# Kernel optimization log

Measured on AMD Instinct MI355X. Metric: run time of the kernel, lower is better.

Reference implementation:

```python
import jax, jax.numpy as jnp
import numpy as np

B, L, D = 2, 1024, 1024
HID, E, K = 2048, 8, 2

def setup_inputs() -> dict:
    key = jax.random.key(0)
    ks = jax.random.split(key, 4)
    std = 0.02
    return {
        "x": jax.random.normal(ks[0], (B, L, D), dtype=jnp.float32),
        "router_scale": jnp.ones((D,), dtype=jnp.float32),
        "router_w": jax.random.normal(ks[1], (D, E), dtype=jnp.float32) * std,
        "gating_w": jax.random.normal(ks[2], (E, 2, HID, D), dtype=jnp.float32) * std,
        "linear_w": jax.random.normal(ks[3], (E, HID, D), dtype=jnp.float32) * std,
        "per_expert_scale": jnp.ones((E,), dtype=jnp.float32),
    }

def reference(x, router_scale, router_w, gating_w, linear_w, per_expert_scale):
    d = x.shape[-1]
    # RMSNorm without scale
    var = jnp.mean(jnp.square(x), axis=-1, keepdims=True)
    r_in = x * jax.lax.rsqrt(var + 1e-6)
    r_in = r_in * jax.lax.rsqrt(jnp.array(d, dtype=r_in.dtype)) * router_scale
    # Router
    logits = jnp.dot(r_in, router_w).astype(jnp.float32)          # [B,L,E]
    probs = jax.nn.softmax(logits, axis=-1)
    _, top_k_idx = jax.lax.top_k(logits, K)                        # [B,L,K]
    indicator = jax.nn.one_hot(top_k_idx, probs.shape[-1], dtype=probs.dtype)  # [B,L,K,E]
    gate_weights = indicator.sum(axis=-2) * probs                  # [B,L,E]
    renorm = jnp.sum(gate_weights, axis=-1, keepdims=True)
    renorm = jnp.where(renorm > 0.0, renorm, 1.0)
    weights = probs / renorm
    top_k_w = jnp.take_along_axis(weights, top_k_idx, axis=-1)     # [B,L,K]
    # Combine weights per expert (indices in top-k are distinct)
    combine = jnp.einsum('blke,blk->ble', indicator, top_k_w)      # [B,L,E]
    combine = combine * per_expert_scale                            # fold per-expert scale
    # Dense all-expert GELU-gated FFN; identical math to per-token gathered weights,
    # since unselected experts get combine weight 0.
    gate0 = jnp.einsum('bld,ehd->bleh', x, gating_w[:, 0])         # [B,L,E,H]
    gate1 = jnp.einsum('bld,ehd->bleh', x, gating_w[:, 1])
    act = jax.nn.gelu(gate0) * gate1                               # approximate gelu, as flax nn.gelu
    out = jnp.einsum('bleh,ehd,ble->bld', act, linear_w, combine)
    return out.astype(x.dtype)
```

## Files before the change

### kernel.cpp

```cpp
#include <hip/hip_runtime.h>
#include <math.h>

#define NB 2
#define NL 1024
#define ND 1024
#define NH 2048
#define NE 8
#define NTOK (NB*NL)
#define NSLOT (NTOK*2)

typedef float f32x4 __attribute__((ext_vector_type(4)));
typedef short s16x8 __attribute__((ext_vector_type(8)));
typedef short s16x4 __attribute__((ext_vector_type(4)));
typedef unsigned u32x4 __attribute__((ext_vector_type(4)));

__device__ __forceinline__ unsigned short f2bf(float f) {
    union { float f; unsigned u; } v; v.f = f;
    unsigned r = v.u + 0x7FFFu + ((v.u >> 16) & 1u);
    return (unsigned short)(r >> 16);
}

__device__ __forceinline__ unsigned pk2(float a, float b) {
    unsigned r;
    asm("v_cvt_pk_bf16_f32 %0, %1, %2" : "=v"(r) : "v"(a), "v"(b));
    return r;
}

__device__ __forceinline__ void gl_lds16(const unsigned short* g, unsigned short* l) {
    __builtin_amdgcn_global_load_lds(
        (const __attribute__((address_space(1))) unsigned int*)(const void*)g,
        (__attribute__((address_space(3))) unsigned int*)(void*)l, 16, 0, 0);
}

__global__ void router_kernel(const float* __restrict__ x,
                              const float* __restrict__ rscale,
                              const float* __restrict__ rw,
                              const float* __restrict__ pes,
                              int* __restrict__ cursor,
                              int* __restrict__ tok_slot,
                              float* __restrict__ w_slot,
                              unsigned short* __restrict__ xb)
{
    const int wave = threadIdx.x >> 6;
    const int lane = threadIdx.x & 63;
    const int t = blockIdx.x * 4 + wave;
    const float* xt = x + (size_t)t * ND;
    unsigned short* xbt = xb + (size_t)t * ND;

    float part[NE];
#pragma unroll
    for (int e = 0; e < NE; ++e) part[e] = 0.f;
    float ss = 0.f;

#pragma unroll
    for (int i = 0; i < 4; ++i) {
        int d = (lane + 64 * i) * 4;
        float4 xv = *(const float4*)(xt + d);
        float4 sv = *(const float4*)(rscale + d);
        s16x4 o;
        o[0] = (short)f2bf(xv.x); o[1] = (short)f2bf(xv.y);
        o[2] = (short)f2bf(xv.z); o[3] = (short)f2bf(xv.w);
        *(s16x4*)(xbt + d) = o;
        float xs[4] = {xv.x, xv.y, xv.z, xv.w};
        float sc[4] = {sv.x, sv.y, sv.z, sv.w};
        const float* rwp = rw + (size_t)d * NE;
#pragma unroll
        for (int c = 0; c < 4; ++c) {
            float v = xs[c];
            ss += v * v;
            float xr = v * sc[c];
            float4 r0 = *(const float4*)(rwp + c * NE);
            float4 r1 = *(const float4*)(rwp + c * NE + 4);
            part[0] += xr * r0.x; part[1] += xr * r0.y;
            part[2] += xr * r0.z; part[3] += xr * r0.w;
            part[4] += xr * r1.x; part[5] += xr * r1.y;
            part[6] += xr * r1.z; part[7] += xr * r1.w;
        }
    }
#pragma unroll
    for (int off = 32; off > 0; off >>= 1) {
        ss += __shfl_xor(ss, off, 64);
#pragma unroll
        for (int e = 0; e < NE; ++e) part[e] += __shfl_xor(part[e], off, 64);
    }
    if (lane == 0) {
        float rinv = rsqrtf(ss * (1.f / ND) + 1e-6f) * rsqrtf((float)ND);
        float lg[NE];
#pragma unroll
        for (int e = 0; e < NE; ++e) lg[e] = part[e] * rinv;
        int i0 = 0; float b0 = lg[0];
#pragma unroll
        for (int e = 1; e < NE; ++e) if (lg[e] > b0) { b0 = lg[e]; i0 = e; }
        int i1 = -1; float b1 = -INFINITY;
#pragma unroll
        for (int e = 0; e < NE; ++e) if (e != i0 && lg[e] > b1) { b1 = lg[e]; i1 = e; }
        float e1 = expf(b1 - b0);
        float denom = 1.f + e1;
        float w0 = pes[i0] / denom;
        float w1 = pes[i1] * e1 / denom;
        int s0 = atomicAdd(&cursor[i0], 1);
        tok_slot[i0 * NTOK + s0] = t; w_slot[i0 * NTOK + s0] = w0;
        int s1 = atomicAdd(&cursor[i1], 1);
        tok_slot[i1 * NTOK + s1] = t; w_slot[i1 * NTOK + s1] = w1;
    }
}

#define TL_BLOCKS ((ND/64)*(NH/64)*NE)
__global__ __launch_bounds__(256) void prep_weights(const float* __restrict__ lw,
                                                    unsigned short* __restrict__ lwT)
{
    const int b2 = blockIdx.x;
    const int tid = threadIdx.x;
    const int d0 = (b2 & 15) * 64;
    const int h0 = ((b2 >> 4) & 31) * 64;
    const int e  = b2 >> 9;
    __shared__ unsigned short T[64][66];
    {
        const int hr = tid >> 2;
        const int dc = (tid & 3) * 16;
        const float* p = lw + ((size_t)e * NH + h0 + hr) * ND + d0 + dc;
        float t[16];
        *(float4*)&t[0]  = *(const float4*)(p);
        *(float4*)&t[4]  = *(const float4*)(p + 4);
        *(float4*)&t[8]  = *(const float4*)(p + 8);
        *(float4*)&t[12] = *(const float4*)(p + 12);
#pragma unroll
        for (int i = 0; i < 8; ++i) {
            unsigned pk = (unsigned)f2bf(t[2 * i]) | ((unsigned)f2bf(t[2 * i + 1]) << 16);
            *(unsigned*)&T[hr][dc + 2 * i] = pk;
        }
    }
    __syncthreads();
    {
        const int dr = tid >> 2;
        const int hc = (tid & 3) * 16;
        s16x8 o0, o1;
#pragma unroll
        for (int i = 0; i < 8; ++i) o0[i] = (short)T[hc + i][dr];
#pragma unroll
        for (int i = 0; i < 8; ++i) o1[i] = (short)T[hc + 8 + i][dr];
        unsigned short* q = lwT + ((size_t)e * ND + d0 + dr) * NH + h0 + hc;
        *(s16x8*)(q)     = o0;
        *(s16x8*)(q + 8) = o1;
    }
}

#define BM 128
#define BH 64
#define BK 32
__global__ __launch_bounds__(256, 3) void gate_gemm(
    const unsigned short* __restrict__ xb, const float* __restrict__ gw,
    const int* __restrict__ cursor,
    const int* __restrict__ tok_slot, const float* __restrict__ w_slot,
    unsigned short* __restrict__ act)
{
    const int e = blockIdx.z;
    const int n = cursor[e];
    const int row0 = blockIdx.y * BM;
    if (row0 >= n) return;
    const int b0 = e * NTOK;
    const int h0 = blockIdx.x * BH;

    __shared__ unsigned short As[BM][BK];
    __shared__ unsigned short Bs[BM][BK];
    __shared__ int toks[BM];
    __shared__ float swv[BM];

    const int tid = threadIdx.x;
    if (tid < BM) {
        int r = row0 + tid;
        toks[tid] = (r < n) ? tok_slot[b0 + r] : 0;
        swv[tid]  = (r < n) ? w_slot[b0 + r] : 0.f;
    }
    __syncthreads();

    const int lane = tid & 63;
    const int wid  = tid >> 6;
    const int wm = wid & 1;
    const int wn = wid >> 1;

    const int drow = lane >> 2;
    const int c8  = (((lane & 3) - ((lane >> 3) & 3)) & 3) * 8;
    const int ar0 = wid * 32 + drow;
    const unsigned short* asrc0 = xb + (size_t)toks[ar0] * ND + c8;
    const unsigned short* asrc1 = xb + (size_t)toks[ar0 + 16] * ND + c8;
    const int br0 = wid * 32 + drow;
    const int br1 = br0 + 16;
    const float* bsrc0 = gw + (((size_t)e * 2 + (br0 >> 6)) * NH + h0 + (br0 & 63)) * ND + c8;
    const float* bsrc1 = gw + (((size_t)e * 2 + (br1 >> 6)) * NH + h0 + (br1 & 63)) * ND + c8;
    unsigned short* bdst0 = &Bs[br0][(lane & 3) * 8];
    unsigned short* bdst1 = &Bs[br1][(lane & 3) * 8];

    f32x4 acc[2][4][2];
#pragma unroll
    for (int gg = 0; gg < 2; ++gg)
#pragma unroll
        for (int i = 0; i < 4; ++i)
#pragma unroll
            for (int j = 0; j < 2; ++j)
                acc[gg][i][j] = (f32x4){0.f, 0.f, 0.f, 0.f};

    const int fr = lane & 15;
    const int pS = (((lane >> 4) + (fr >> 1)) & 3) * 8;

    for (int k0 = 0; k0 < ND; k0 += BK) {
        f32x4 b00 = *(const f32x4*)(bsrc0 + k0);
        f32x4 b01 = *(const f32x4*)(bsrc0 + k0 + 4);
        f32x4 b10 = *(const f32x4*)(bsrc1 + k0);
        f32x4 b11 = *(const f32x4*)(bsrc1 + k0 + 4);
        gl_lds16(asrc0 + k0, &As[wid * 32][0]);
        gl_lds16(asrc1 + k0, &As[wid * 32 + 16][0]);
        u32x4 w0, w1;
        w0[0] = pk2(b00[0], b00[1]); w0[1] = pk2(b00[2], b00[3]);
        w0[2] = pk2(b01[0], b01[1]); w0[3] = pk2(b01[2], b01[3]);
        w1[0] = pk2(b10[0], b10[1]); w1[1] = pk2(b10[2], b10[3]);
        w1[2] = pk2(b11[0], b11[1]); w1[3] = pk2(b11[2], b11[3]);
        *(u32x4*)bdst0 = w0;
        *(u32x4*)bdst1 = w1;
        __syncthreads();

        s16x8 af[4], bfr[2][2];
#pragma unroll
        for (int i = 0; i < 4; ++i)
            af[i] = *(const s16x8*)&As[wm * 64 + i * 16 + fr][pS];
#pragma unroll
        for (int gg = 0; gg < 2; ++gg)
#pragma unroll
            for (int j = 0; j < 2; ++j)
                bfr[gg][j] = *(const s16x8*)&Bs[gg * 64 + wn * 32 + j * 16 + fr][pS];
#pragma unroll
        for (int gg = 0; gg < 2; ++gg)
#pragma unroll
            for (int i = 0; i < 4; ++i)
#pragma unroll
                for (int j = 0; j < 2; ++j)
                    acc[gg][i][j] = __builtin_amdgcn_mfma_f32_16x16x32_bf16(
                        af[i], bfr[gg][j], acc[gg][i][j], 0, 0, 0);
        __syncthreads();
    }

    const int rb = (lane >> 4) * 4;
#pragma unroll
    for (int i = 0; i < 4; ++i)
#pragma unroll
        for (int r = 0; r < 4; ++r) {
            int ml = wm * 64 + i * 16 + rb + r;
            int rr = row0 + ml;
            if (rr < n) {
                float w = swv[ml];
#pragma unroll
                for (int j = 0; j < 2; ++j) {
                    float g0v = acc[0][i][j][r];
                    float g1v = acc[1][i][j][r];
                    float u = 0.7978845608028654f * (g0v + 0.044715f * g0v * g0v * g0v);
                    float ex = __expf(2.f * u);
                    float th = 1.f - 2.f / (ex + 1.f);
                    float a = 0.5f * g0v * (1.f + th) * g1v * w;
                    act[(size_t)(b0 + rr) * NH + (h0 + wn * 32 + j * 16 + fr)] = f2bf(a);
                }
            }
        }
}

#define DBM 128
#define DBN 128
#define DBK 32
#define KSPLIT 2
#define KC (NH / KSPLIT)
__global__ __launch_bounds__(256, 3) void down_gemm(
    const unsigned short* __restrict__ act, const unsigned short* __restrict__ lwT,
    const int* __restrict__ cursor,
    const int* __restrict__ tok_slot, float* __restrict__ out)
{
    const int e  = blockIdx.z >> 1;
    const int kc = blockIdx.z & 1;
    const int n = cursor[e];
    const int row0 = blockIdx.y * DBM;
    if (row0 >= n) return;
    const int b0 = e * NTOK;
    const int d0 = blockIdx.x * DBN;

    __shared__ unsigned short As[DBM][DBK];
    __shared__ unsigned short Bs[DBN][DBK];
    __shared__ int stok[DBM];

    const int tid = threadIdx.x;
    if (tid < DBM) {
        int r = row0 + tid;
        stok[tid] = (r < n) ? tok_slot[b0 + r] : 0;
    }
    __syncthreads();

    const int lane = tid & 63;
    const int wid  = tid >> 6;
    const int wm = wid & 1;
    const int wn = wid >> 1;

    const int drow = lane >> 2;
    const int c8  = (((lane & 3) - ((lane >> 3) & 3)) & 3) * 8;
    const int ar0 = wid * 32 + drow;
    const int rr0 = row0 + ar0, rr1 = rr0 + 16;
    const int sl0 = b0 + (rr0 < n ? rr0 : 0);
    const int sl1 = b0 + (rr1 < n ? rr1 : 0);
    const unsigned short* asrc0 = act + (size_t)sl0 * NH + kc * KC + c8;
    const unsigned short* asrc1 = act + (size_t)sl1 * NH + kc * KC + c8;
    const unsigned short* bsrc0 = lwT + ((size_t)e * ND + d0 + ar0) * NH + kc * KC + c8;
    const unsigned short* bsrc1 = bsrc0 + 16 * NH;

    f32x4 acc[4][4];
#pragma unroll
    for (int i = 0; i < 4; ++i)
#pragma unroll
        for (int j = 0; j < 4; ++j)
            acc[i][j] = (f32x4){0.f, 0.f, 0.f, 0.f};

    const int fr = lane & 15;
    const int pS = (((lane >> 4) + (fr >> 1)) & 3) * 8;

    for (int k0 = 0; k0 < KC; k0 += DBK) {
        gl_lds16(asrc0 + k0, &As[wid * 32][0]);
        gl_lds16(asrc1 + k0, &As[wid * 32 + 16][0]);
        gl_lds16(bsrc0 + k0, &Bs[wid * 32][0]);
        gl_lds16(bsrc1 + k0, &Bs[wid * 32 + 16][0]);
        __syncthreads();

        s16x8 af[4], bfr[4];
#pragma unroll
        for (int i = 0; i < 4; ++i)
            af[i] = *(const s16x8*)&As[wm * 64 + i * 16 + fr][pS];
#pragma unroll
        for (int j = 0; j < 4; ++j)
            bfr[j] = *(const s16x8*)&Bs[wn * 64 + j * 16 + fr][pS];
#pragma unroll
        for (int i = 0; i < 4; ++i)
#pragma unroll
            for (int j = 0; j < 4; ++j)
                acc[i][j] = __builtin_amdgcn_mfma_f32_16x16x32_bf16(af[i], bfr[j], acc[i][j], 0, 0, 0);
        __syncthreads();
    }

    const int rb = (lane >> 4) * 4;
#pragma unroll
    for (int i = 0; i < 4; ++i)
#pragma unroll
        for (int r = 0; r < 4; ++r) {
            int ml = wm * 64 + i * 16 + rb + r;
            int rr = row0 + ml;
            if (rr < n) {
                int tok = stok[ml];
#pragma unroll
                for (int j = 0; j < 4; ++j)
                    atomicAdd(&out[(size_t)tok * ND + d0 + wn * 64 + j * 16 + fr],
                              acc[i][j][r]);
            }
        }
}

extern "C" void kernel_launch(void* const* d_in, const int* in_sizes, int n_in,
                              void* d_out, int out_size, void* d_ws, size_t ws_size,
                              hipStream_t stream)
{
    const float* x      = (const float*)d_in[0];
    const float* rscale = (const float*)d_in[1];
    const float* rw     = (const float*)d_in[2];
    const float* gw     = (const float*)d_in[3];
    const float* lw     = (const float*)d_in[4];
    const float* pes    = (const float*)d_in[5];
    float* out = (float*)d_out;

    char* ws = (char*)d_ws;
    int* cursor = (int*)ws;
    int*   tok_slot      = (int*)(ws + 128);
    float* w_slot        = (float*)(ws + 65664);
    unsigned short* xb   = (unsigned short*)(ws + 131200);
    unsigned short* act  = (unsigned short*)(ws + 4325504);
    unsigned short* lwT  = (unsigned short*)(ws + 71434368);

    hipMemsetAsync(d_ws, 0, 128, stream);
    hipMemsetAsync(d_out, 0, (size_t)out_size * sizeof(float), stream);

    router_kernel<<<NTOK / 4, 256, 0, stream>>>(x, rscale, rw, pes, cursor,
                                                tok_slot, w_slot, xb);

    prep_weights<<<TL_BLOCKS, 256, 0, stream>>>(lw, lwT);

    dim3 g2(NH / BH, NTOK / BM, NE);
    gate_gemm<<<g2, 256, 0, stream>>>(xb, gw, cursor, tok_slot, w_slot, act);

    dim3 g3(ND / DBN, NTOK / DBM, NE * KSPLIT);
    down_gemm<<<g3, 256, 0, stream>>>(act, lwT, cursor, tok_slot, out);
}
```

Baseline: 429.8 us.

## Double-buffer LDS tiles in gate and down GEMMs to overlap loads with MFMA

Both grouped GEMM kernels now keep two LDS buffers for the A and B tiles. The next K-tile is fetched (global-to-LDS for activations, register-staged fp32-to-bf16 conversion for gate weights) while the MFMAs run on the current tile, which removes one barrier per iteration. Launch bounds are raised from 3 to 4 waves per SIMD to push occupancy. The cost is doubled LDS use and more register pressure, which may limit achievable occupancy or cause spills.

```diff
diff --git a/kernel.cpp b/kernel.cpp
--- a/kernel.cpp
+++ b/kernel.cpp
@@ -148,7 +148,7 @@
 #define BM 128
 #define BH 64
 #define BK 32
-__global__ __launch_bounds__(256, 3) void gate_gemm(
+__global__ __launch_bounds__(256, 4) void gate_gemm(
     const unsigned short* __restrict__ xb, const float* __restrict__ gw,
     const int* __restrict__ cursor,
     const int* __restrict__ tok_slot, const float* __restrict__ w_slot,
@@ -161,8 +161,8 @@
     const int b0 = e * NTOK;
     const int h0 = blockIdx.x * BH;
 
-    __shared__ unsigned short As[BM][BK];
-    __shared__ unsigned short Bs[BM][BK];
+    __shared__ unsigned short As[2][BM][BK];
+    __shared__ unsigned short Bs[2][BM][BK];
     __shared__ int toks[BM];
     __shared__ float swv[BM];
 
@@ -188,8 +188,7 @@
     const int br1 = br0 + 16;
     const float* bsrc0 = gw + (((size_t)e * 2 + (br0 >> 6)) * NH + h0 + (br0 & 63)) * ND + c8;
     const float* bsrc1 = gw + (((size_t)e * 2 + (br1 >> 6)) * NH + h0 + (br1 & 63)) * ND + c8;
-    unsigned short* bdst0 = &Bs[br0][(lane & 3) * 8];
-    unsigned short* bdst1 = &Bs[br1][(lane & 3) * 8];
+    const int bc = (lane & 3) * 8;
 
     f32x4 acc[2][4][2];
 #pragma unroll
@@ -203,31 +202,50 @@
     const int fr = lane & 15;
     const int pS = (((lane >> 4) + (fr >> 1)) & 3) * 8;
 
-    for (int k0 = 0; k0 < ND; k0 += BK) {
-        f32x4 b00 = *(const f32x4*)(bsrc0 + k0);
-        f32x4 b01 = *(const f32x4*)(bsrc0 + k0 + 4);
-        f32x4 b10 = *(const f32x4*)(bsrc1 + k0);
-        f32x4 b11 = *(const f32x4*)(bsrc1 + k0 + 4);
-        gl_lds16(asrc0 + k0, &As[wid * 32][0]);
-        gl_lds16(asrc1 + k0, &As[wid * 32 + 16][0]);
+    const int NT = ND / BK;
+
+    {
+        f32x4 b00 = *(const f32x4*)(bsrc0);
+        f32x4 b01 = *(const f32x4*)(bsrc0 + 4);
+        f32x4 b10 = *(const f32x4*)(bsrc1);
+        f32x4 b11 = *(const f32x4*)(bsrc1 + 4);
+        gl_lds16(asrc0, &As[0][wid * 32][0]);
+        gl_lds16(asrc1, &As[0][wid * 32 + 16][0]);
         u32x4 w0, w1;
         w0[0] = pk2(b00[0], b00[1]); w0[1] = pk2(b00[2], b00[3]);
         w0[2] = pk2(b01[0], b01[1]); w0[3] = pk2(b01[2], b01[3]);
         w1[0] = pk2(b10[0], b10[1]); w1[1] = pk2(b10[2], b10[3]);
         w1[2] = pk2(b11[0], b11[1]); w1[3] = pk2(b11[2], b11[3]);
-        *(u32x4*)bdst0 = w0;
-        *(u32x4*)bdst1 = w1;
-        __syncthreads();
+        *(u32x4*)&Bs[0][br0][bc] = w0;
+        *(u32x4*)&Bs[0][br1][bc] = w1;
+    }
+    __syncthreads();
+
+    for (int t = 0; t < NT; ++t) {
+        const int cur = t & 1;
+        const int nxt = cur ^ 1;
+        const int k1 = (t + 1) * BK;
+        const bool more = (t + 1 < NT);
+
+        f32x4 n00, n01, n10, n11;
+        if (more) {
+            n00 = *(const f32x4*)(bsrc0 + k1);
+            n01 = *(const f32x4*)(bsrc0 + k1 + 4);
+            n10 = *(const f32x4*)(bsrc1 + k1);
+            n11 = *(const f32x4*)(bsrc1 + k1 + 4);
+            gl_lds16(asrc0 + k1, &As[nxt][wid * 32][0]);
+            gl_lds16(asrc1 + k1, &As[nxt][wid * 32 + 16][0]);
+        }
 
         s16x8 af[4], bfr[2][2];
 #pragma unroll
         for (int i = 0; i < 4; ++i)
-            af[i] = *(const s16x8*)&As[wm * 64 + i * 16 + fr][pS];
+            af[i] = *(const s16x8*)&As[cur][wm * 64 + i * 16 + fr][pS];
 #pragma unroll
         for (int gg = 0; gg < 2; ++gg)
 #pragma unroll
             for (int j = 0; j < 2; ++j)
-                bfr[gg][j] = *(const s16x8*)&Bs[gg * 64 + wn * 32 + j * 16 + fr][pS];
+                bfr[gg][j] = *(const s16x8*)&Bs[cur][gg * 64 + wn * 32 + j * 16 + fr][pS];
 #pragma unroll
         for (int gg = 0; gg < 2; ++gg)
 #pragma unroll
@@ -236,6 +254,16 @@
                 for (int j = 0; j < 2; ++j)
                     acc[gg][i][j] = __builtin_amdgcn_mfma_f32_16x16x32_bf16(
                         af[i], bfr[gg][j], acc[gg][i][j], 0, 0, 0);
+
+        if (more) {
+            u32x4 w0, w1;
+            w0[0] = pk2(n00[0], n00[1]); w0[1] = pk2(n00[2], n00[3]);
+            w0[2] = pk2(n01[0], n01[1]); w0[3] = pk2(n01[2], n01[3]);
+            w1[0] = pk2(n10[0], n10[1]); w1[1] = pk2(n10[2], n10[3]);
+            w1[2] = pk2(n11[0], n11[1]); w1[3] = pk2(n11[2], n11[3]);
+            *(u32x4*)&Bs[nxt][br0][bc] = w0;
+            *(u32x4*)&Bs[nxt][br1][bc] = w1;
+        }
         __syncthreads();
     }
 
@@ -267,7 +295,7 @@
 #define DBK 32
 #define KSPLIT 2
 #define KC (NH / KSPLIT)
-__global__ __launch_bounds__(256, 3) void down_gemm(
+__global__ __launch_bounds__(256, 4) void down_gemm(
     const unsigned short* __restrict__ act, const unsigned short* __restrict__ lwT,
     const int* __restrict__ cursor,
     const int* __restrict__ tok_slot, float* __restrict__ out)
@@ -280,8 +308,8 @@
     const int b0 = e * NTOK;
     const int d0 = blockIdx.x * DBN;
 
-    __shared__ unsigned short As[DBM][DBK];
-    __shared__ unsigned short Bs[DBN][DBK];
+    __shared__ unsigned short As[2][DBM][DBK];
+    __shared__ unsigned short Bs[2][DBN][DBK];
     __shared__ int stok[DBM];
 
     const int tid = threadIdx.x;
@@ -317,20 +345,32 @@
     const int fr = lane & 15;
     const int pS = (((lane >> 4) + (fr >> 1)) & 3) * 8;
 
-    for (int k0 = 0; k0 < KC; k0 += DBK) {
-        gl_lds16(asrc0 + k0, &As[wid * 32][0]);
-        gl_lds16(asrc1 + k0, &As[wid * 32 + 16][0]);
-        gl_lds16(bsrc0 + k0, &Bs[wid * 32][0]);
-        gl_lds16(bsrc1 + k0, &Bs[wid * 32 + 16][0]);
-        __syncthreads();
+    const int NT = KC / DBK;
+
+    gl_lds16(asrc0, &As[0][wid * 32][0]);
+    gl_lds16(asrc1, &As[0][wid * 32 + 16][0]);
+    gl_lds16(bsrc0, &Bs[0][wid * 32][0]);
+    gl_lds16(bsrc1, &Bs[0][wid * 32 + 16][0]);
+    __syncthreads();
+
+    for (int t = 0; t < NT; ++t) {
+        const int cur = t & 1;
+        const int nxt = cur ^ 1;
+        const int k1 = (t + 1) * DBK;
+        if (t + 1 < NT) {
+            gl_lds16(asrc0 + k1, &As[nxt][wid * 32][0]);
+            gl_lds16(asrc1 + k1, &As[nxt][wid * 32 + 16][0]);
+            gl_lds16(bsrc0 + k1, &Bs[nxt][wid * 32][0]);
+            gl_lds16(bsrc1 + k1, &Bs[nxt][wid * 32 + 16][0]);
+        }
 
         s16x8 af[4], bfr[4];
 #pragma unroll
         for (int i = 0; i < 4; ++i)
-            af[i] = *(const s16x8*)&As[wm * 64 + i * 16 + fr][pS];
+            af[i] = *(const s16x8*)&As[cur][wm * 64 + i * 16 + fr][pS];
 #pragma unroll
         for (int j = 0; j < 4; ++j)
-            bfr[j] = *(const s16x8*)&Bs[wn * 64 + j * 16 + fr][pS];
+            bfr[j] = *(const s16x8*)&Bs[cur][wn * 64 + j * 16 + fr][pS];
 #pragma unroll
         for (int i = 0; i < 4; ++i)
 #pragma unroll
```

After: 418.4 us. 2.7% less time.

## Double-buffer LDS in both expert GEMMs and replace atomics with partial-sum gather

Applied to the files above, without the earlier changes.

Both gate and down GEMMs switch from direct global-to-LDS loads with a single buffer to register-staged, double-buffered LDS tiles, so global loads for the next K tile overlap MFMA work on the current one. The down GEMM no longer atomically adds into the output. It writes per-slot, per-K-split partial results into a workspace buffer, and a new gather kernel sums the four partials per token using a token-to-slot map recorded by the router. This removes the output memset and the float atomics, at the cost of extra register pressure, a larger workspace (about 128 MB of partials), and an additional launch.

```diff
diff --git a/kernel.cpp b/kernel.cpp
--- a/kernel.cpp
+++ b/kernel.cpp
@@ -26,12 +26,6 @@
     return r;
 }
 
-__device__ __forceinline__ void gl_lds16(const unsigned short* g, unsigned short* l) {
-    __builtin_amdgcn_global_load_lds(
-        (const __attribute__((address_space(1))) unsigned int*)(const void*)g,
-        (__attribute__((address_space(3))) unsigned int*)(void*)l, 16, 0, 0);
-}
-
 __global__ void router_kernel(const float* __restrict__ x,
                               const float* __restrict__ rscale,
                               const float* __restrict__ rw,
@@ -39,6 +33,7 @@
                               int* __restrict__ cursor,
                               int* __restrict__ tok_slot,
                               float* __restrict__ w_slot,
+                              int2* __restrict__ t2s,
                               unsigned short* __restrict__ xb)
 {
     const int wave = threadIdx.x >> 6;
@@ -102,6 +97,7 @@
         tok_slot[i0 * NTOK + s0] = t; w_slot[i0 * NTOK + s0] = w0;
         int s1 = atomicAdd(&cursor[i1], 1);
         tok_slot[i1 * NTOK + s1] = t; w_slot[i1 * NTOK + s1] = w1;
+        t2s[t] = make_int2(i0 * NTOK + s0, i1 * NTOK + s1);
     }
 }
 
@@ -148,6 +144,48 @@
 #define BM 128
 #define BH 64
 #define BK 32
+
+#define G_ISSUE(Sa0,Sa1,Sb0,Sb1,Sb2,Sb3,k) do { \
+    Sa0 = *(const s16x8*)(asrc0 + (k)); \
+    Sa1 = *(const s16x8*)(asrc1 + (k)); \
+    Sb0 = *(const f32x4*)(bsrc0 + (k)); \
+    Sb1 = *(const f32x4*)(bsrc0 + (k) + 4); \
+    Sb2 = *(const f32x4*)(bsrc1 + (k)); \
+    Sb3 = *(const f32x4*)(bsrc1 + (k) + 4); \
+} while(0)
+
+#define G_WRITE(P,Sa0,Sa1,Sb0,Sb1,Sb2,Sb3) do { \
+    *(s16x8*)&As[P][arow][acol]      = Sa0; \
+    *(s16x8*)&As[P][arow + 16][acol] = Sa1; \
+    u32x4 w0_, w1_; \
+    w0_[0] = pk2(Sb0[0],Sb0[1]); w0_[1] = pk2(Sb0[2],Sb0[3]); \
+    w0_[2] = pk2(Sb1[0],Sb1[1]); w0_[3] = pk2(Sb1[2],Sb1[3]); \
+    w1_[0] = pk2(Sb2[0],Sb2[1]); w1_[1] = pk2(Sb2[2],Sb2[3]); \
+    w1_[2] = pk2(Sb3[0],Sb3[1]); w1_[3] = pk2(Sb3[2],Sb3[3]); \
+    *(u32x4*)&Bs[P][arow][acol]      = w0_; \
+    *(u32x4*)&Bs[P][arow + 16][acol] = w1_; \
+} while(0)
+
+#define G_COMPUTE(P) do { \
+    s16x8 af[4], bfr[2][2]; \
+    _Pragma("unroll") \
+    for (int i_ = 0; i_ < 4; ++i_) \
+        af[i_] = *(const s16x8*)&As[P][wm * 64 + i_ * 16 + fr][pS]; \
+    _Pragma("unroll") \
+    for (int g_ = 0; g_ < 2; ++g_) \
+        _Pragma("unroll") \
+        for (int j_ = 0; j_ < 2; ++j_) \
+            bfr[g_][j_] = *(const s16x8*)&Bs[P][g_ * 64 + wn * 32 + j_ * 16 + fr][pS]; \
+    _Pragma("unroll") \
+    for (int g_ = 0; g_ < 2; ++g_) \
+        _Pragma("unroll") \
+        for (int i_ = 0; i_ < 4; ++i_) \
+            _Pragma("unroll") \
+            for (int j_ = 0; j_ < 2; ++j_) \
+                acc[g_][i_][j_] = __builtin_amdgcn_mfma_f32_16x16x32_bf16( \
+                    af[i_], bfr[g_][j_], acc[g_][i_][j_], 0, 0, 0); \
+} while(0)
+
 __global__ __launch_bounds__(256, 3) void gate_gemm(
     const unsigned short* __restrict__ xb, const float* __restrict__ gw,
     const int* __restrict__ cursor,
@@ -161,8 +199,8 @@
     const int b0 = e * NTOK;
     const int h0 = blockIdx.x * BH;
 
-    __shared__ unsigned short As[BM][BK];
-    __shared__ unsigned short Bs[BM][BK];
+    __shared__ unsigned short As[2][BM][BK];
+    __shared__ unsigned short Bs[2][BM][BK];
     __shared__ int toks[BM];
     __shared__ float swv[BM];
 
@@ -181,15 +219,13 @@
 
     const int drow = lane >> 2;
     const int c8  = (((lane & 3) - ((lane >> 3) & 3)) & 3) * 8;
-    const int ar0 = wid * 32 + drow;
-    const unsigned short* asrc0 = xb + (size_t)toks[ar0] * ND + c8;
-    const unsigned short* asrc1 = xb + (size_t)toks[ar0 + 16] * ND + c8;
-    const int br0 = wid * 32 + drow;
-    const int br1 = br0 + 16;
-    const float* bsrc0 = gw + (((size_t)e * 2 + (br0 >> 6)) * NH + h0 + (br0 & 63)) * ND + c8;
+    const int arow = wid * 32 + drow;
+    const int acol = (lane & 3) * 8;
+    const unsigned short* asrc0 = xb + (size_t)toks[arow] * ND + c8;
+    const unsigned short* asrc1 = xb + (size_t)toks[arow + 16] * ND + c8;
+    const int br1 = arow + 16;
+    const float* bsrc0 = gw + (((size_t)e * 2 + (arow >> 6)) * NH + h0 + (arow & 63)) * ND + c8;
     const float* bsrc1 = gw + (((size_t)e * 2 + (br1 >> 6)) * NH + h0 + (br1 & 63)) * ND + c8;
-    unsigned short* bdst0 = &Bs[br0][(lane & 3) * 8];
-    unsigned short* bdst1 = &Bs[br1][(lane & 3) * 8];
 
     f32x4 acc[2][4][2];
 #pragma unroll
@@ -203,39 +239,24 @@
     const int fr = lane & 15;
     const int pS = (((lane >> 4) + (fr >> 1)) & 3) * 8;
 
-    for (int k0 = 0; k0 < ND; k0 += BK) {
-        f32x4 b00 = *(const f32x4*)(bsrc0 + k0);
-        f32x4 b01 = *(const f32x4*)(bsrc0 + k0 + 4);
-        f32x4 b10 = *(const f32x4*)(bsrc1 + k0);
-        f32x4 b11 = *(const f32x4*)(bsrc1 + k0 + 4);
-        gl_lds16(asrc0 + k0, &As[wid * 32][0]);
-        gl_lds16(asrc1 + k0, &As[wid * 32 + 16][0]);
-        u32x4 w0, w1;
-        w0[0] = pk2(b00[0], b00[1]); w0[1] = pk2(b00[2], b00[3]);
-        w0[2] = pk2(b01[0], b01[1]); w0[3] = pk2(b01[2], b01[3]);
-        w1[0] = pk2(b10[0], b10[1]); w1[1] = pk2(b10[2], b10[3]);
-        w1[2] = pk2(b11[0], b11[1]); w1[3] = pk2(b11[2], b11[3]);
-        *(u32x4*)bdst0 = w0;
-        *(u32x4*)bdst1 = w1;
+    const int NT = ND / BK;
+
+    s16x8 xa0, xa1, ya0, ya1;
+    f32x4 xb0, xb1, xb2, xb3, yb0, yb1, yb2, yb3;
+
+    G_ISSUE(xa0, xa1, xb0, xb1, xb2, xb3, 0);
+    G_ISSUE(ya0, ya1, yb0, yb1, yb2, yb3, BK);
+    G_WRITE(0, xa0, xa1, xb0, xb1, xb2, xb3);
+    __syncthreads();
+
+    for (int t = 0; t < NT; t += 2) {
+        if (t + 2 < NT) G_ISSUE(xa0, xa1, xb0, xb1, xb2, xb3, (t + 2) * BK);
+        G_COMPUTE(0);
+        G_WRITE(1, ya0, ya1, yb0, yb1, yb2, yb3);
         __syncthreads();
-
-        s16x8 af[4], bfr[2][2];
-#pragma unroll
-        for (int i = 0; i < 4; ++i)
-            af[i] = *(const s16x8*)&As[wm * 64 + i * 16 + fr][pS];
-#pragma unroll
-        for (int gg = 0; gg < 2; ++gg)
-#pragma unroll
-            for (int j = 0; j < 2; ++j)
-                bfr[gg][j] = *(const s16x8*)&Bs[gg * 64 + wn * 32 + j * 16 + fr][pS];
-#pragma unroll
-        for (int gg = 0; gg < 2; ++gg)
-#pragma unroll
-            for (int i = 0; i < 4; ++i)
-#pragma unroll
-                for (int j = 0; j < 2; ++j)
-                    acc[gg][i][j] = __builtin_amdgcn_mfma_f32_16x16x32_bf16(
-                        af[i], bfr[gg][j], acc[gg][i][j], 0, 0, 0);
+        if (t + 3 < NT) G_ISSUE(ya0, ya1, yb0, yb1, yb2, yb3, (t + 3) * BK);
+        G_COMPUTE(1);
+        if (t + 2 < NT) G_WRITE(0, xa0, xa1, xb0, xb1, xb2, xb3);
         __syncthreads();
     }
 
@@ -267,10 +288,41 @@
 #define DBK 32
 #define KSPLIT 2
 #define KC (NH / KSPLIT)
+
+#define D_ISSUE(Sa0,Sa1,Sb0,Sb1,k) do { \
+    Sa0 = *(const s16x8*)(asrc0 + (k)); \
+    Sa1 = *(const s16x8*)(asrc1 + (k)); \
+    Sb0 = *(const s16x8*)(bsrc0 + (k)); \
+    Sb1 = *(const s16x8*)(bsrc1 + (k)); \
+} while(0)
+
+#define D_WRITE(P,Sa0,Sa1,Sb0,Sb1) do { \
+    *(s16x8*)&As[P][arow][acol]      = Sa0; \
+    *(s16x8*)&As[P][arow + 16][acol] = Sa1; \
+    *(s16x8*)&Bs[P][arow][acol]      = Sb0; \
+    *(s16x8*)&Bs[P][arow + 16][acol] = Sb1; \
+} while(0)
+
+#define D_COMPUTE(P) do { \
+    s16x8 af[4], bfr[4]; \
+    _Pragma("unroll") \
+    for (int i_ = 0; i_ < 4; ++i_) \
+        af[i_] = *(const s16x8*)&As[P][wm * 64 + i_ * 16 + fr][pS]; \
+    _Pragma("unroll") \
+    for (int j_ = 0; j_ < 4; ++j_) \
+        bfr[j_] = *(const s16x8*)&Bs[P][wn * 64 + j_ * 16 + fr][pS]; \
+    _Pragma("unroll") \
+    for (int i_ = 0; i_ < 4; ++i_) \
+        _Pragma("unroll") \
+        for (int j_ = 0; j_ < 4; ++j_) \
+            acc[i_][j_] = __builtin_amdgcn_mfma_f32_16x16x32_bf16( \
+                af[i_], bfr[j_], acc[i_][j_], 0, 0, 0); \
+} while(0)
+
 __global__ __launch_bounds__(256, 3) void down_gemm(
     const unsigned short* __restrict__ act, const unsigned short* __restrict__ lwT,
     const int* __restrict__ cursor,
-    const int* __restrict__ tok_slot, float* __restrict__ out)
+    const int* __restrict__ tok_slot, float* __restrict__ partial)
 {
     const int e  = blockIdx.z >> 1;
     const int kc = blockIdx.z & 1;
@@ -280,17 +332,10 @@
     const int b0 = e * NTOK;
     const int d0 = blockIdx.x * DBN;
 
-    __shared__ unsigned short As[DBM][DBK];
-    __shared__ unsigned short Bs[DBN][DBK];
-    __shared__ int stok[DBM];
+    __shared__ unsigned short As[2][DBM][DBK];
+    __shared__ unsigned short Bs[2][DBN][DBK];
 
     const int tid = threadIdx.x;
-    if (tid < DBM) {
-        int r = row0 + tid;
-        stok[tid] = (r < n) ? tok_slot[b0 + r] : 0;
-    }
-    __syncthreads();
-
     const int lane = tid & 63;
     const int wid  = tid >> 6;
     const int wm = wid & 1;
@@ -298,13 +343,14 @@
 
     const int drow = lane >> 2;
     const int c8  = (((lane & 3) - ((lane >> 3) & 3)) & 3) * 8;
-    const int ar0 = wid * 32 + drow;
-    const int rr0 = row0 + ar0, rr1 = rr0 + 16;
+    const int arow = wid * 32 + drow;
+    const int acol = (lane & 3) * 8;
+    const int rr0 = row0 + arow, rr1 = rr0 + 16;
     const int sl0 = b0 + (rr0 < n ? rr0 : 0);
     const int sl1 = b0 + (rr1 < n ? rr1 : 0);
     const unsigned short* asrc0 = act + (size_t)sl0 * NH + kc * KC + c8;
     const unsigned short* asrc1 = act + (size_t)sl1 * NH + kc * KC + c8;
-    const unsigned short* bsrc0 = lwT + ((size_t)e * ND + d0 + ar0) * NH + kc * KC + c8;
+    const unsigned short* bsrc0 = lwT + ((size_t)e * ND + d0 + arow) * NH + kc * KC + c8;
     const unsigned short* bsrc1 = bsrc0 + 16 * NH;
 
     f32x4 acc[4][4];
@@ -317,28 +363,29 @@
     const int fr = lane & 15;
     const int pS = (((lane >> 4) + (fr >> 1)) & 3) * 8;
 
-    for (int k0 = 0; k0 < KC; k0 += DBK) {
-        gl_lds16(asrc0 + k0, &As[wid * 32][0]);
-        gl_lds16(asrc1 + k0, &As[wid * 32 + 16][0]);
-        gl_lds16(bsrc0 + k0, &Bs[wid * 32][0]);
-        gl_lds16(bsrc1 + k0, &Bs[wid * 32 + 16][0]);
+    const int NT = KC / DBK;
+
+    s16x8 xa0, xa1, xb0, xb1;
+    s16x8 ya0, ya1, yb0, yb1;
+
+    G_UNUSED_SEMI:;
+    D_ISSUE(xa0, xa1, xb0, xb1, 0);
+    D_ISSUE(ya0, ya1, yb0, yb1, DBK);
+    D_WRITE(0, xa0, xa1, xb0, xb1);
+    __syncthreads();
+
+    for (int t = 0; t < NT; t += 2) {
+        if (t + 2 < NT) D_ISSUE(xa0, xa1, xb0, xb1, (t + 2) * DBK);
+        D_COMPUTE(0);
+        D_WRITE(1, ya0, ya1, yb0, yb1);
         __syncthreads();
-
-        s16x8 af[4], bfr[4];
-#pragma unroll
-        for (int i = 0; i < 4; ++i)
-            af[i] = *(const s16x8*)&As[wm * 64 + i * 16 + fr][pS];
-#pragma unroll
-        for (int j = 0; j < 4; ++j)
-            bfr[j] = *(const s16x8*)&Bs[wn * 64 + j * 16 + fr][pS];
-#pragma unroll
-        for (int i = 0; i < 4; ++i)
-#pragma unroll
-            for (int j = 0; j < 4; ++j)
-                acc[i][j] = __builtin_amdgcn_mfma_f32_16x16x32_bf16(af[i], bfr[j], acc[i][j], 0, 0, 0);
+        if (t + 3 < NT) D_ISSUE(ya0, ya1, yb0, yb1, (t + 3) * DBK);
+        D_COMPUTE(1);
+        if (t + 2 < NT) D_WRITE(0, xa0, xa1, xb0, xb1);
         __syncthreads();
     }
 
+    float* prt = partial + ((size_t)kc * (NE * NTOK)) * ND;
     const int rb = (lane >> 4) * 4;
 #pragma unroll
     for (int i = 0; i < 4; ++i)
@@ -347,13 +394,31 @@
             int ml = wm * 64 + i * 16 + rb + r;
             int rr = row0 + ml;
             if (rr < n) {
-                int tok = stok[ml];
 #pragma unroll
                 for (int j = 0; j < 4; ++j)
-                    atomicAdd(&out[(size_t)tok * ND + d0 + wn * 64 + j * 16 + fr],
-                              acc[i][j][r]);
+                    prt[(size_t)(b0 + rr) * ND + d0 + wn * 64 + j * 16 + fr] = acc[i][j][r];
             }
         }
+}
+
+__global__ __launch_bounds__(256) void gather_out(const float* __restrict__ partial,
+                                                  const int2* __restrict__ t2s,
+                                                  float* __restrict__ out)
+{
+    const int t = blockIdx.x;
+    const int2 ss = t2s[t];
+    const size_t plane = (size_t)(NE * NTOK) * ND;
+    const float* p00 = partial + (size_t)ss.x * ND;
+    const float* p01 = p00 + plane;
+    const float* p10 = partial + (size_t)ss.y * ND;
+    const float* p11 = p10 + plane;
+    const int d = threadIdx.x * 4;
+    f32x4 a = *(const f32x4*)(p00 + d);
+    f32x4 b = *(const f32x4*)(p01 + d);
+    f32x4 c = *(const f32x4*)(p10 + d);
+    f32x4 e = *(const f32x4*)(p11 + d);
+    f32x4 v = a + b + c + e;
+    *(f32x4*)(out + (size_t)t * ND + d) = v;
 }
 
 extern "C" void kernel_launch(void* const* d_in, const int* in_sizes, int n_in,
@@ -372,15 +437,16 @@
     int* cursor = (int*)ws;
     int*   tok_slot      = (int*)(ws + 128);
     float* w_slot        = (float*)(ws + 65664);
-    unsigned short* xb   = (unsigned short*)(ws + 131200);
-    unsigned short* act  = (unsigned short*)(ws + 4325504);
-    unsigned short* lwT  = (unsigned short*)(ws + 71434368);
+    int2*  t2s           = (int2*)(ws + 131200);
+    unsigned short* xb   = (unsigned short*)(ws + 147584);
+    unsigned short* act  = (unsigned short*)(ws + 4341888);
+    unsigned short* lwT  = (unsigned short*)(ws + 71450752);
+    float* partial       = (float*)(ws + 105005184);
 
     hipMemsetAsync(d_ws, 0, 128, stream);
-    hipMemsetAsync(d_out, 0, (size_t)out_size * sizeof(float), stream);
 
     router_kernel<<<NTOK / 4, 256, 0, stream>>>(x, rscale, rw, pes, cursor,
-                                                tok_slot, w_slot, xb);
+                                                tok_slot, w_slot, t2s, xb);
 
     prep_weights<<<TL_BLOCKS, 256, 0, stream>>>(lw, lwT);
 
@@ -388,5 +454,7 @@
     gate_gemm<<<g2, 256, 0, stream>>>(xb, gw, cursor, tok_slot, w_slot, act);
 
     dim3 g3(ND / DBN, NTOK / DBM, NE * KSPLIT);
-    down_gemm<<<g3, 256, 0, stream>>>(act, lwT, cursor, tok_slot, out);
-}
+    down_gemm<<<g3, 256, 0, stream>>>(act, lwT, cursor, tok_slot, partial);
+
+    gather_out<<<NTOK, 256, 0, stream>>>(partial, t2s, out);
+}
```

Measured after the change: 406.2 us. 1.06x faster.
